# Kernel tuning notes

Hardware: AMD Instinct MI355X
Metric: run time of the kernel (lower is better)

Reference implementation:

```python
import jax, jax.numpy as jnp
import numpy as np

N, E = 50000, 640000
D_IN, D_OUT, N_BASES = 128, 128, 8


def setup_inputs() -> dict:
    key = jax.random.key(0)
    k1, k2, k3, k4, k5, k6 = jax.random.split(key, 6)
    x = jax.random.normal(k1, (N, D_IN), dtype=jnp.float32)
    edge_index = jax.random.randint(k2, (2, E), 0, N, dtype=jnp.int64)
    # basis-decomposed relation weights (num_relations=1)
    bases = jax.random.normal(k3, (N_BASES, D_IN, D_OUT), dtype=jnp.float32) * 0.05
    comp = jax.random.normal(k4, (1, N_BASES), dtype=jnp.float32)
    root = jax.random.normal(k5, (D_IN, D_OUT), dtype=jnp.float32) * 0.05
    bias = jax.random.normal(k6, (D_OUT,), dtype=jnp.float32) * 0.01
    return {"x": x, "edge_index": edge_index, "bases": bases,
            "comp": comp, "root": root, "bias": bias}


def reference(x, edge_index, bases, comp, root, bias):
    # W[rel=0] = sum_b comp[0,b] * bases[b]  -> [D_IN, D_OUT]
    W = jnp.einsum('b,bio->io', comp[0], bases)
    src = edge_index[0]  # message sources (x_j)
    dst = edge_index[1]  # aggregation targets
    # gather -> scatter-add (aggr='add'), then relation-specific transform
    agg = jax.ops.segment_sum(x[src], dst, num_segments=x.shape[0])  # [N, D_IN]
    out = agg @ W + x @ root + bias  # root/self-loop transform + bias
    return out
```

## Files before the change

kernel.cpp:

```cpp
#include <hip/hip_runtime.h>

#define N_NODES 50000
#define N_EDGES 640000
#define D 128
#define NB 8
#define PAD 32
#define NSTRIP 3125
#define GRID_G 1024

typedef _Float16 half_t;
typedef __attribute__((ext_vector_type(8))) _Float16 half8;
typedef __attribute__((ext_vector_type(4))) float f32x4;

__global__ __launch_bounds__(256)
void init_kernel(const float* __restrict__ bases,
                 const float* __restrict__ comp,
                 const float* __restrict__ root,
                 half_t* __restrict__ Wt,
                 half_t* __restrict__ Rt,
                 int* __restrict__ cnt) {
    int i = blockIdx.x * 256 + threadIdx.x;
    if (i < N_NODES) cnt[i] = 0;
    if (i < D * D) {
        int ii = i >> 7, o = i & 127;
        float acc = 0.f;
#pragma unroll
        for (int b = 0; b < NB; ++b)
            acc += comp[b] * bases[((size_t)b * D + ii) * D + o];
        Wt[o * D + ii] = (half_t)acc;
        Rt[o * D + ii] = (half_t)root[i];
    }
}

__global__ __launch_bounds__(256, 4)
void gemm_kernel(const float* __restrict__ x,
                 const half_t* __restrict__ Wt,
                 const half_t* __restrict__ Rt,
                 const float* __restrict__ bias,
                 half_t* __restrict__ y,
                 float* __restrict__ out) {
    const int tid  = threadIdx.x;
    const int wave = tid >> 6;
    const int lane = tid & 63;
    const int m    = lane & 15;
    const int quad = lane >> 4;
    const int gw   = blockIdx.x * 4 + wave;
    const int q    = gw & 3;
    const int s0   = gw >> 2;
    const int SSTR = GRID_G;

    half8 bw[2][4], br[2][4];
    float bb[2];
#pragma unroll
    for (int t = 0; t < 2; ++t) {
        const int nt = 2 * q + t;
        const half_t* wp = Wt + (nt * 16 + m) * D + quad * 8;
        const half_t* rp = Rt + (nt * 16 + m) * D + quad * 8;
#pragma unroll
        for (int kk = 0; kk < 4; ++kk) {
            bw[t][kk] = *(const half8*)(wp + kk * 32);
            br[t][kk] = *(const half8*)(rp + kk * 32);
        }
        bb[t] = bias[nt * 16 + m];
    }

    const float4* x4 = (const float4*)x;
    for (int s = s0; s < NSTRIP; s += SSTR) {
        size_t ab = (size_t)(s * 16 + m) * 32 + quad * 2;
        half8 a[4];
#pragma unroll
        for (int kk = 0; kk < 4; ++kk) {
            float4 v0 = x4[ab + kk * 8];
            float4 v1 = x4[ab + kk * 8 + 1];
            half8 h;
            h[0] = (half_t)v0.x; h[1] = (half_t)v0.y; h[2] = (half_t)v0.z; h[3] = (half_t)v0.w;
            h[4] = (half_t)v1.x; h[5] = (half_t)v1.y; h[6] = (half_t)v1.z; h[7] = (half_t)v1.w;
            a[kk] = h;
        }

        f32x4 accW[2], accR[2];
#pragma unroll
        for (int t = 0; t < 2; ++t) {
            accW[t] = (f32x4){0.f, 0.f, 0.f, 0.f};
            accR[t] = (f32x4){0.f, 0.f, 0.f, 0.f};
        }
#pragma unroll
        for (int t = 0; t < 2; ++t)
#pragma unroll
            for (int kk = 0; kk < 4; ++kk) {
                accW[t] = __builtin_amdgcn_mfma_f32_16x16x32_f16(a[kk], bw[t][kk], accW[t], 0, 0, 0);
                accR[t] = __builtin_amdgcn_mfma_f32_16x16x32_f16(a[kk], br[t][kk], accR[t], 0, 0, 0);
            }

#pragma unroll
        for (int t = 0; t < 2; ++t) {
            int col = (2 * q + t) * 16 + m;
#pragma unroll
            for (int r = 0; r < 4; ++r) {
                int row = s * 16 + quad * 4 + r;
                y[(size_t)row * D + col]   = (half_t)accW[t][r];
                out[(size_t)row * D + col] = accR[t][r] + bb[t];
            }
        }
    }
}

__global__ __launch_bounds__(256)
void bucket_kernel(const int* __restrict__ eidx,
                   const half_t* __restrict__ y,
                   float* __restrict__ out,
                   int* __restrict__ cnt,
                   int* __restrict__ bucket) {
    int e = blockIdx.x * 256 + threadIdx.x;
    if (e >= N_EDGES) return;
    int src = eidx[e];
    int dst = eidx[N_EDGES + e];
    int pos = atomicAdd(&cnt[dst], 1);
    if (pos < PAD) {
        bucket[(size_t)dst * PAD + pos] = src;
    } else {
        const half_t* yr = y + (size_t)src * D;
        float* op = out + (size_t)dst * D;
        for (int q = 0; q < D; ++q) atomicAdd(op + q, (float)yr[q]);
    }
}

__global__ __launch_bounds__(256)
void gather_kernel(const int* __restrict__ cnt,
                   const int* __restrict__ bucket,
                   const half_t* __restrict__ y,
                   float* __restrict__ out) {
    int node = blockIdx.x * 16 + (threadIdx.x >> 4);
    int q = threadIdx.x & 15;
    if (node >= N_NODES) return;
    int c = cnt[node];
    if (c > PAD) c = PAD;
    const int* b = bucket + (size_t)node * PAD;
    float acc[8] = {0.f, 0.f, 0.f, 0.f, 0.f, 0.f, 0.f, 0.f};
    int i = 0;
    for (; i + 8 <= c; i += 8) {
        int4 s0 = *(const int4*)(b + i);
        int4 s1 = *(const int4*)(b + i + 4);
        half8 v0 = *(const half8*)(y + (size_t)s0.x * D + q * 8);
        half8 v1 = *(const half8*)(y + (size_t)s0.y * D + q * 8);
        half8 v2 = *(const half8*)(y + (size_t)s0.z * D + q * 8);
        half8 v3 = *(const half8*)(y + (size_t)s0.w * D + q * 8);
        half8 v4 = *(const half8*)(y + (size_t)s1.x * D + q * 8);
        half8 v5 = *(const half8*)(y + (size_t)s1.y * D + q * 8);
        half8 v6 = *(const half8*)(y + (size_t)s1.z * D + q * 8);
        half8 v7 = *(const half8*)(y + (size_t)s1.w * D + q * 8);
#pragma unroll
        for (int j = 0; j < 8; ++j)
            acc[j] += ((float)v0[j] + (float)v1[j]) + ((float)v2[j] + (float)v3[j])
                    + ((float)v4[j] + (float)v5[j]) + ((float)v6[j] + (float)v7[j]);
    }
    for (; i + 4 <= c; i += 4) {
        int4 s = *(const int4*)(b + i);
        half8 v0 = *(const half8*)(y + (size_t)s.x * D + q * 8);
        half8 v1 = *(const half8*)(y + (size_t)s.y * D + q * 8);
        half8 v2 = *(const half8*)(y + (size_t)s.z * D + q * 8);
        half8 v3 = *(const half8*)(y + (size_t)s.w * D + q * 8);
#pragma unroll
        for (int j = 0; j < 8; ++j)
            acc[j] += ((float)v0[j] + (float)v1[j]) + ((float)v2[j] + (float)v3[j]);
    }
    for (; i < c; ++i) {
        half8 v = *(const half8*)(y + (size_t)b[i] * D + q * 8);
#pragma unroll
        for (int j = 0; j < 8; ++j) acc[j] += (float)v[j];
    }
    float4* op = (float4*)(out + (size_t)node * D + q * 8);
    float4 o0 = op[0], o1 = op[1];
    o0.x += acc[0]; o0.y += acc[1]; o0.z += acc[2]; o0.w += acc[3];
    o1.x += acc[4]; o1.y += acc[5]; o1.z += acc[6]; o1.w += acc[7];
    op[0] = o0; op[1] = o1;
}

extern "C" void kernel_launch(void* const* d_in, const int* in_sizes, int n_in,
                              void* d_out, int out_size, void* d_ws, size_t ws_size,
                              hipStream_t stream) {
    const float* x     = (const float*)d_in[0];
    const int*   eidx  = (const int*)d_in[1];
    const float* bases = (const float*)d_in[2];
    const float* comp  = (const float*)d_in[3];
    const float* root  = (const float*)d_in[4];
    const float* bias  = (const float*)d_in[5];
    float* out = (float*)d_out;

    char* ws = (char*)d_ws;
    half_t* y      = (half_t*)ws;
    half_t* Wt     = (half_t*)(ws + 12800000);
    half_t* Rt     = (half_t*)(ws + 12832768);
    int*    cnt    = (int*)   (ws + 12865536);
    int*    bucket = (int*)   (ws + 13065536);

    init_kernel<<<(N_NODES + 255) / 256, 256, 0, stream>>>(
        bases, comp, root, Wt, Rt, cnt);
    gemm_kernel<<<GRID_G, 256, 0, stream>>>(
        x, Wt, Rt, bias, y, out);
    bucket_kernel<<<(N_EDGES + 255) / 256, 256, 0, stream>>>(
        eidx, y, out, cnt, bucket);
    gather_kernel<<<(N_NODES + 15) / 16, 256, 0, stream>>>(
        cnt, bucket, y, out);
}
```

Baseline: 170.4 us.

## Fuse edge bucketing and GEMM into one kernel with split block roles

Merges the bucket kernel and the GEMM kernel into a single launch. The first 256 blocks bucket edges by destination while the remaining 768 blocks compute the two node transforms, so the atomic-heavy bucketing overlaps with the MFMA work. Bucket overflow edges no longer do 128 scalar float atomics each. They go to an overflow list that the gather kernel scans linearly for nodes whose count exceeds the pad. This saves a launch and hides bucketing latency, but the overflow scan costs O(novf) per overflowing node, and GEMM work per block changes.

```diff
diff --git a/kernel.cpp b/kernel.cpp
--- a/kernel.cpp
+++ b/kernel.cpp
@@ -6,7 +6,9 @@
 #define NB 8
 #define PAD 32
 #define NSTRIP 3125
-#define GRID_G 1024
+
+#define BUCKET_B 256
+#define GEMM_B   768
 
 typedef _Float16 half_t;
 typedef __attribute__((ext_vector_type(8))) _Float16 half8;
@@ -18,8 +20,10 @@
                  const float* __restrict__ root,
                  half_t* __restrict__ Wt,
                  half_t* __restrict__ Rt,
-                 int* __restrict__ cnt) {
+                 int* __restrict__ cnt,
+                 int* __restrict__ novf) {
     int i = blockIdx.x * 256 + threadIdx.x;
+    if (i == 0) *novf = 0;
     if (i < N_NODES) cnt[i] = 0;
     if (i < D * D) {
         int ii = i >> 7, o = i & 127;
@@ -33,21 +37,44 @@
 }
 
 __global__ __launch_bounds__(256, 4)
-void gemm_kernel(const float* __restrict__ x,
-                 const half_t* __restrict__ Wt,
-                 const half_t* __restrict__ Rt,
-                 const float* __restrict__ bias,
-                 half_t* __restrict__ y,
-                 float* __restrict__ out) {
-    const int tid  = threadIdx.x;
+void fused_kernel(const float* __restrict__ x,
+                  const half_t* __restrict__ Wt,
+                  const half_t* __restrict__ Rt,
+                  const float* __restrict__ bias,
+                  const int* __restrict__ eidx,
+                  half_t* __restrict__ y,
+                  float* __restrict__ out,
+                  int* __restrict__ cnt,
+                  int* __restrict__ bucket,
+                  int* __restrict__ ovf,
+                  int* __restrict__ novf) {
+    const int tid = threadIdx.x;
+
+    if (blockIdx.x < BUCKET_B) {
+        int t = blockIdx.x * 256 + tid;
+        for (int e = t; e < N_EDGES; e += BUCKET_B * 256) {
+            int src = eidx[e];
+            int dst = eidx[N_EDGES + e];
+            int pos = atomicAdd(&cnt[dst], 1);
+            if (pos < PAD) {
+                bucket[(size_t)dst * PAD + pos] = src;
+            } else {
+                int k = atomicAdd(novf, 1);
+                ovf[2 * k]     = src;
+                ovf[2 * k + 1] = dst;
+            }
+        }
+        return;
+    }
+
+    const int gb   = blockIdx.x - BUCKET_B;
     const int wave = tid >> 6;
     const int lane = tid & 63;
     const int m    = lane & 15;
     const int quad = lane >> 4;
-    const int gw   = blockIdx.x * 4 + wave;
-    const int q    = gw & 3;
-    const int s0   = gw >> 2;
-    const int SSTR = GRID_G;
+    const int q    = wave;
+    const int s0   = gb;
+    const int SSTR = GEMM_B;
 
     half8 bw[2][4], br[2][4];
     float bb[2];
@@ -106,35 +133,17 @@
 }
 
 __global__ __launch_bounds__(256)
-void bucket_kernel(const int* __restrict__ eidx,
-                   const half_t* __restrict__ y,
-                   float* __restrict__ out,
-                   int* __restrict__ cnt,
-                   int* __restrict__ bucket) {
-    int e = blockIdx.x * 256 + threadIdx.x;
-    if (e >= N_EDGES) return;
-    int src = eidx[e];
-    int dst = eidx[N_EDGES + e];
-    int pos = atomicAdd(&cnt[dst], 1);
-    if (pos < PAD) {
-        bucket[(size_t)dst * PAD + pos] = src;
-    } else {
-        const half_t* yr = y + (size_t)src * D;
-        float* op = out + (size_t)dst * D;
-        for (int q = 0; q < D; ++q) atomicAdd(op + q, (float)yr[q]);
-    }
-}
-
-__global__ __launch_bounds__(256)
 void gather_kernel(const int* __restrict__ cnt,
                    const int* __restrict__ bucket,
                    const half_t* __restrict__ y,
+                   const int* __restrict__ ovf,
+                   const int* __restrict__ novf,
                    float* __restrict__ out) {
     int node = blockIdx.x * 16 + (threadIdx.x >> 4);
     int q = threadIdx.x & 15;
     if (node >= N_NODES) return;
-    int c = cnt[node];
-    if (c > PAD) c = PAD;
+    int c_raw = cnt[node];
+    int c = c_raw > PAD ? PAD : c_raw;
     const int* b = bucket + (size_t)node * PAD;
     float acc[8] = {0.f, 0.f, 0.f, 0.f, 0.f, 0.f, 0.f, 0.f};
     int i = 0;
@@ -169,6 +178,16 @@
 #pragma unroll
         for (int j = 0; j < 8; ++j) acc[j] += (float)v[j];
     }
+    if (c_raw > PAD) {
+        int n = *novf;
+        for (int k = 0; k < n; ++k) {
+            if (ovf[2 * k + 1] == node) {
+                half8 v = *(const half8*)(y + (size_t)ovf[2 * k] * D + q * 8);
+#pragma unroll
+                for (int j = 0; j < 8; ++j) acc[j] += (float)v[j];
+            }
+        }
+    }
     float4* op = (float4*)(out + (size_t)node * D + q * 8);
     float4 o0 = op[0], o1 = op[1];
     o0.x += acc[0]; o0.y += acc[1]; o0.z += acc[2]; o0.w += acc[3];
@@ -193,13 +212,13 @@
     half_t* Rt     = (half_t*)(ws + 12832768);
     int*    cnt    = (int*)   (ws + 12865536);
     int*    bucket = (int*)   (ws + 13065536);
+    int*    novf   = (int*)   (ws + 19465536);
+    int*    ovf    = (int*)   (ws + 19465552);
 
     init_kernel<<<(N_NODES + 255) / 256, 256, 0, stream>>>(
-        bases, comp, root, Wt, Rt, cnt);
-    gemm_kernel<<<GRID_G, 256, 0, stream>>>(
-        x, Wt, Rt, bias, y, out);
-    bucket_kernel<<<(N_EDGES + 255) / 256, 256, 0, stream>>>(
-        eidx, y, out, cnt, bucket);
+        bases, comp, root, Wt, Rt, cnt, novf);
+    fused_kernel<<<BUCKET_B + GEMM_B, 256, 0, stream>>>(
+        x, Wt, Rt, bias, eidx, y, out, cnt, bucket, ovf, novf);
     gather_kernel<<<(N_NODES + 15) / 16, 256, 0, stream>>>(
-        cnt, bucket, y, out);
-}
+        cnt, bucket, y, ovf, novf, out);
+}
```

After: 148.1 us. 1.15x faster.
